# Kernel tuning notes

Measured on AMD Instinct MI355X. Metric: run time of the kernel, lower is better.

## Reference

```python
import jax, jax.numpy as jnp
import numpy as np

B, L, DM, H, DK, DV = 4, 1024, 1024, 16, 64, 64


def setup_inputs() -> dict:
    key = jax.random.key(0)
    ks = jax.random.split(key, 9)
    s = 0.02
    q = jax.random.normal(ks[0], (B, L, DM), jnp.float32)
    k = jax.random.normal(ks[1], (B, L, DM), jnp.float32)
    v = jax.random.normal(ks[2], (B, L, DM), jnp.float32)
    # causal mask: True = masked out
    attn_mask = jnp.broadcast_to(jnp.triu(jnp.ones((L, L), bool), k=1), (B, L, L))
    w_q = jax.random.normal(ks[3], (DM, H * DK), jnp.float32) * s
    w_k = jax.random.normal(ks[4], (DM, H * DK), jnp.float32) * s
    w_v = jax.random.normal(ks[5], (DM, H * DV), jnp.float32) * s
    w_o = jax.random.normal(ks[6], (H * DV, DM), jnp.float32) * s
    ln_g = jnp.ones((DM,), jnp.float32)
    ln_b = jnp.zeros((DM,), jnp.float32)
    return {"q": q, "k": k, "v": v, "w_q": w_q, "w_k": w_k, "w_v": w_v,
            "w_o": w_o, "ln_g": ln_g, "ln_b": ln_b,
            "attn_mask": attn_mask, "n_head": H}


def _mha(q, k, v, w_q, w_k, w_v, w_o, ln_g, ln_b, attn_mask, n_head):
    b, lq, dm = q.shape
    lk = k.shape[1]
    d_k = w_q.shape[1] // n_head
    d_v = w_v.shape[1] // n_head
    temper = jnp.asarray(np.sqrt(dm), q.dtype)  # NOTE: sqrt(d_model), as in source
    residual = q
    # faithful to source: flat .view reshape (b, l, h*d) -> (b*h, l, d), NO transpose
    qh = (q @ w_q).reshape(b * n_head, lq, d_k)
    kh = (k @ w_k).reshape(b * n_head, lk, d_k)
    vh = (v @ w_v).reshape(b * n_head, lk, d_v)
    attn = jnp.einsum('bqd,bkd->bqk', qh, kh) / temper  # (b*h, lq, lk)
    mask_r = jnp.tile(attn_mask, (n_head, 1, 1))
    attn = jnp.where(mask_r, -jnp.inf, attn)
    attn = jax.nn.softmax(attn, axis=-1)
    out = jnp.einsum('bqk,bkd->bqd', attn, vh)  # (b*h, lq, d_v)
    out = out.reshape(b, lq, n_head * d_v)
    out = out @ w_o + residual  # dropout = identity (eval)
    mu = jnp.mean(out, axis=-1, keepdims=True)
    var = jnp.mean(jnp.square(out - mu), axis=-1, keepdims=True)
    out = (out - mu) * jax.lax.rsqrt(var + 1e-6) * ln_g + ln_b
    return out, attn


def reference(q, k, v, w_q, w_k, w_v, w_o, ln_g, ln_b, attn_mask, n_head):
    return _mha(q, k, v, w_q, w_k, w_v, w_o, ln_g, ln_b, attn_mask, n_head)
```

## Files before the change

### kernel.cpp

```cpp
#include <hip/hip_runtime.h>
#include <stdint.h>

typedef unsigned short u16;
typedef __attribute__((ext_vector_type(8))) short bf16x8;
typedef __attribute__((ext_vector_type(4))) float f32x4;
typedef __attribute__((ext_vector_type(4))) unsigned short us4;

#define MFMA_BF16(a, b, c) __builtin_amdgcn_mfma_f32_16x16x32_bf16((a), (b), (c), 0, 0, 0)

__device__ __forceinline__ u16 f2bf(float f) {
  uint32_t u = __builtin_bit_cast(uint32_t, f);
  u += 0x7fffu + ((u >> 16) & 1u);
  return (u16)(u >> 16);
}

__device__ __forceinline__ void async_copy16(void* lds, const void* g) {
  __builtin_amdgcn_global_load_lds(
      (const __attribute__((address_space(1))) unsigned int*)g,
      (__attribute__((address_space(3))) unsigned int*)lds, 16, 0, 0);
}

__global__ __launch_bounds__(256) void k_cast3(const float4* __restrict__ q,
                                               const float4* __restrict__ k,
                                               const float4* __restrict__ v,
                                               us4* __restrict__ dst) {
  const float4* src = (blockIdx.y == 0) ? q : ((blockIdx.y == 1) ? k : v);
  int i = blockIdx.x * 256 + threadIdx.x;
  float4 val = src[i];
  us4 o;
  o[0] = f2bf(val.x); o[1] = f2bf(val.y); o[2] = f2bf(val.z); o[3] = f2bf(val.w);
  dst[(size_t)blockIdx.y * 1048576 + i] = o;
}

__global__ __launch_bounds__(256) void k_wtrans4(const float* __restrict__ w0,
                                                 const float* __restrict__ w1,
                                                 const float* __restrict__ w2,
                                                 const float* __restrict__ w3,
                                                 u16* __restrict__ dstbase) {
  const float* W = (blockIdx.z == 0) ? w0 : (blockIdx.z == 1) ? w1
                   : (blockIdx.z == 2) ? w2 : w3;
  u16* WT = dstbase + (size_t)blockIdx.z * 1048576;
  __shared__ float t[32][33];
  int bx = blockIdx.x, by = blockIdx.y;
  int tid = threadIdx.x;
  int c = tid & 31, r0 = tid >> 5;
#pragma unroll
  for (int i = 0; i < 4; ++i) {
    int r = r0 + i * 8;
    t[r][c] = W[(size_t)(by * 32 + r) * 1024 + bx * 32 + c];
  }
  __syncthreads();
#pragma unroll
  for (int i = 0; i < 4; ++i) {
    int r = r0 + i * 8;
    WT[(size_t)(bx * 32 + r) * 1024 + by * 32 + c] = f2bf(t[c][r]);
  }
}

__global__ __launch_bounds__(256) void k_vtrans(const u16* __restrict__ VP, u16* __restrict__ VT) {
  int jt = blockIdx.x;
  int bh = blockIdx.y;
  __shared__ u16 t[64][65];
  int tid = threadIdx.x;
  const u16* src = VP + (size_t)bh * 65536 + (size_t)jt * 64 * 64;
#pragma unroll
  for (int i = 0; i < 16; ++i) {
    int e = tid + i * 256;
    t[e >> 6][e & 63] = src[e];
  }
  __syncthreads();
  u16* dst = VT + (size_t)bh * 65536 + jt * 64;
#pragma unroll
  for (int i = 0; i < 16; ++i) {
    int e = tid + i * 256;
    int d = e >> 6, j = e & 63;
    dst[(size_t)d * 1024 + j] = t[j][d];
  }
}

__global__ __launch_bounds__(256) void k_gemm_bt(const u16* __restrict__ A,
                                                 const u16* __restrict__ BT,
                                                 u16* __restrict__ Cb, float* __restrict__ Cf,
                                                 const float* __restrict__ res,
                                                 int N, int K, int mode, int wgrp) {
  __shared__ __align__(16) u16 As[2][4096];
  __shared__ __align__(16) u16 Bs[2][4096];
  int bm, bn;
  {
    int wg = blockIdx.x + blockIdx.y * gridDim.x;
    int per = gridDim.y >> 3;
    int xcd = wg & 7;
    int idx = wg >> 3;
    bm = xcd * per + (idx % per);
    bn = idx / per;
  }
  int tid = threadIdx.x;
  int wave = tid >> 6, lane = tid & 63;
  int wr = wave >> 1, wc = wave & 1;
  int fl = lane & 15, fg = lane >> 4;
  f32x4 acc[4][4] = {};

  const char* Abase = (const char*)(A + (size_t)bm * 128 * K);
  const char* Bbase = (const char*)(BT + (wgrp ? (size_t)(bm >> 5) * 1048576 : 0) +
                                    (size_t)bn * 128 * K);
  int off = wave * 1024 + lane * 16;

#define GSTAGE(buf, kt)                                                              \
  {                                                                                  \
    _Pragma("unroll") for (int is = 0; is < 2; ++is) {                               \
      int o = is * 4096 + off;                                                       \
      int row = o >> 6, cb = o & 63;                                                 \
      async_copy16((char*)As[buf] + is * 4096 + wave * 1024,                         \
                   Abase + (size_t)row * (K * 2) + (kt) * 2 + cb);                   \
      async_copy16((char*)Bs[buf] + is * 4096 + wave * 1024,                         \
                   Bbase + (size_t)row * (K * 2) + (kt) * 2 + cb);                   \
    }                                                                                \
  }

  GSTAGE(0, 0);
  __syncthreads();
  int cur = 0;
  for (int kt = 0; kt < K; kt += 32) {
    if (kt + 32 < K) GSTAGE(cur ^ 1, kt + 32);
    bf16x8 af[4], bfr[4];
#pragma unroll
    for (int m = 0; m < 4; ++m)
      af[m] = *(const bf16x8*)((const char*)As[cur] + (wr * 64 + m * 16 + fl) * 64 + fg * 16);
#pragma unroll
    for (int n = 0; n < 4; ++n)
      bfr[n] = *(const bf16x8*)((const char*)Bs[cur] + (wc * 64 + n * 16 + fl) * 64 + fg * 16);
#pragma unroll
    for (int m = 0; m < 4; ++m)
#pragma unroll
      for (int n = 0; n < 4; ++n)
        acc[m][n] = MFMA_BF16(af[m], bfr[n], acc[m][n]);
    __syncthreads();
    cur ^= 1;
  }
#undef GSTAGE

#pragma unroll
  for (int m = 0; m < 4; ++m)
#pragma unroll
    for (int n = 0; n < 4; ++n)
#pragma unroll
      for (int r = 0; r < 4; ++r) {
        int row = bm * 128 + wr * 64 + m * 16 + fg * 4 + r;
        int col = bn * 128 + wc * 64 + n * 16 + fl;
        float v = acc[m][n][r];
        if (mode)
          Cf[(size_t)row * N + col] = v + res[(size_t)row * N + col];
        else
          Cb[(size_t)row * N + col] = f2bf(v);
      }
}

__global__ __launch_bounds__(256) void k_attn(const u16* __restrict__ QP,
                                              const u16* __restrict__ KP,
                                              const u16* __restrict__ VT,
                                              float* __restrict__ attn,
                                              u16* __restrict__ AO) {
  int bh = blockIdx.x;
  int qb = 15 - blockIdx.y;
  int tid = threadIdx.x;
  int wave = tid >> 6, lane = tid & 63;
  int fl = lane & 15, fg = lane >> 4;
  int qw = qb * 64 + wave * 16;

  const u16* Qb = QP + (size_t)bh * 65536;
  const char* Kbyte = (const char*)(KP + (size_t)bh * 65536);
  const u16* Vb = VT + (size_t)bh * 65536;
  float* Ab = attn + (size_t)bh * 1048576;

  __shared__ __align__(16) u16 Ks[2][4096];
  __shared__ __align__(16) float Ps[4][16][68];
  __shared__ __align__(16) u16 Pt[4][16][64];

#define KSTAGE(buf, jt)                                                               \
  {                                                                                   \
    _Pragma("unroll") for (int c2 = 0; c2 < 2; ++c2) {                                \
      int o = c2 * 4096 + wave * 1024 + lane * 16;                                    \
      int row = o >> 7, col = o & 127;                                                \
      async_copy16((char*)Ks[buf] + c2 * 4096 + wave * 1024,                          \
                   Kbyte + (size_t)((jt) * 64 + row) * 128 + (col ^ ((row & 7) << 4))); \
    }                                                                                 \
  }

  bf16x8 qf0 = *(const bf16x8*)(Qb + (size_t)(qw + fl) * 64 + fg * 8);
  bf16x8 qf1 = *(const bf16x8*)(Qb + (size_t)(qw + fl) * 64 + 32 + fg * 8);

  float den[4] = {0.f, 0.f, 0.f, 0.f};

  KSTAGE(0, 0);
  __syncthreads();
  int cur = 0;
  for (int jt = 0; jt <= qb; ++jt) {
    if (jt < qb) KSTAGE(cur ^ 1, jt + 1);
    int j0 = jt * 64;
    f32x4 c[4] = {};
#pragma unroll
    for (int n = 0; n < 4; ++n) {
      int r = n * 16 + fl;
      bf16x8 k0 = *(const bf16x8*)((const char*)Ks[cur] + r * 128 + ((fg * 16) ^ ((r & 7) << 4)));
      bf16x8 k1 = *(const bf16x8*)((const char*)Ks[cur] + r * 128 + ((64 + fg * 16) ^ ((r & 7) << 4)));
      c[n] = MFMA_BF16(qf0, k0, c[n]);
      c[n] = MFMA_BF16(qf1, k1, c[n]);
    }
#pragma unroll
    for (int r = 0; r < 4; ++r) {
      int row = qw + fg * 4 + r;
      float sum = 0.f;
#pragma unroll
      for (int n = 0; n < 4; ++n) {
        int col = j0 + n * 16 + fl;
        float e = (col > row) ? 0.f : __expf(c[n][r] * 0.03125f);
        sum += e;
      }
#pragma unroll
      for (int o2 = 1; o2 < 16; o2 <<= 1) sum += __shfl_xor(sum, o2);
      den[r] += sum;
    }
    __syncthreads();
    cur ^= 1;
  }

  float invden[4];
#pragma unroll
  for (int r = 0; r < 4; ++r) invden[r] = 1.0f / den[r];

  f32x4 oacc[4] = {};

  KSTAGE(0, 0);
  __syncthreads();
  cur = 0;
  for (int jt = 0; jt <= qb; ++jt) {
    if (jt < qb) KSTAGE(cur ^ 1, jt + 1);
    int j0 = jt * 64;
    f32x4 c[4] = {};
#pragma unroll
    for (int n = 0; n < 4; ++n) {
      int r = n * 16 + fl;
      bf16x8 k0 = *(const bf16x8*)((const char*)Ks[cur] + r * 128 + ((fg * 16) ^ ((r & 7) << 4)));
      bf16x8 k1 = *(const bf16x8*)((const char*)Ks[cur] + r * 128 + ((64 + fg * 16) ^ ((r & 7) << 4)));
      c[n] = MFMA_BF16(qf0, k0, c[n]);
      c[n] = MFMA_BF16(qf1, k1, c[n]);
    }
#pragma unroll
    for (int r = 0; r < 4; ++r) {
      int row = qw + fg * 4 + r;
      int lr = fg * 4 + r;
#pragma unroll
      for (int n = 0; n < 4; ++n) {
        int col = j0 + n * 16 + fl;
        float p = (col > row) ? 0.f : __expf(c[n][r] * 0.03125f) * invden[r];
        Ps[wave][lr][n * 16 + fl] = p;
        Pt[wave][lr][n * 16 + fl] = f2bf(p);
      }
    }
    bf16x8 pa0 = *(const bf16x8*)(&Pt[wave][fl][fg * 8]);
    bf16x8 pa1 = *(const bf16x8*)(&Pt[wave][fl][32 + fg * 8]);
#pragma unroll
    for (int n = 0; n < 4; ++n) {
      const u16* vp = Vb + (size_t)(n * 16 + fl) * 1024 + j0;
      bf16x8 v0 = *(const bf16x8*)(vp + fg * 8);
      bf16x8 v1 = *(const bf16x8*)(vp + 32 + fg * 8);
      oacc[n] = MFMA_BF16(pa0, v0, oacc[n]);
      oacc[n] = MFMA_BF16(pa1, v1, oacc[n]);
    }
#pragma unroll
    for (int i = 0; i < 4; ++i) {
      int idx = i * 64 + lane;
      int r16 = idx >> 4, f4 = idx & 15;
      float4 val = *(const float4*)(&Ps[wave][r16][f4 * 4]);
      *(float4*)(Ab + (size_t)(qw + r16) * 1024 + j0 + f4 * 4) = val;
    }
    __syncthreads();
    cur ^= 1;
  }
#undef KSTAGE

  float4 z; z.x = 0.f; z.y = 0.f; z.z = 0.f; z.w = 0.f;
  for (int jt = qb + 1; jt < 16; ++jt) {
    int j0 = jt * 64;
#pragma unroll
    for (int i = 0; i < 4; ++i) {
      int idx = i * 64 + lane;
      int r16 = idx >> 4, f4 = idx & 15;
      *(float4*)(Ab + (size_t)(qw + r16) * 1024 + j0 + f4 * 4) = z;
    }
  }

#pragma unroll
  for (int n = 0; n < 4; ++n)
#pragma unroll
    for (int r = 0; r < 4; ++r)
      AO[(size_t)bh * 65536 + (size_t)(qw + fg * 4 + r) * 64 + n * 16 + fl] = f2bf(oacc[n][r]);
}

__global__ __launch_bounds__(256) void k_lnorm(float* __restrict__ io,
                                               const float* __restrict__ g,
                                               const float* __restrict__ b) {
  int row = blockIdx.x, tid = threadIdx.x;
  float* p = io + (size_t)row * 1024 + tid * 4;
  float4 x = *(const float4*)p;
  float s1 = x.x + x.y + x.z + x.w;
  float s2 = x.x * x.x + x.y * x.y + x.z * x.z + x.w * x.w;
#pragma unroll
  for (int o = 1; o < 64; o <<= 1) {
    s1 += __shfl_xor(s1, o);
    s2 += __shfl_xor(s2, o);
  }
  __shared__ float r1[4], r2[4];
  int wave = tid >> 6;
  if ((tid & 63) == 0) { r1[wave] = s1; r2[wave] = s2; }
  __syncthreads();
  s1 = r1[0] + r1[1] + r1[2] + r1[3];
  s2 = r2[0] + r2[1] + r2[2] + r2[3];
  float mu = s1 * (1.0f / 1024.0f);
  float var = s2 * (1.0f / 1024.0f) - mu * mu;
  float rs = rsqrtf(var + 1e-6f);
  float4 gg = *(const float4*)(g + tid * 4);
  float4 bb = *(const float4*)(b + tid * 4);
  float4 y;
  y.x = (x.x - mu) * rs * gg.x + bb.x;
  y.y = (x.y - mu) * rs * gg.y + bb.y;
  y.z = (x.z - mu) * rs * gg.z + bb.z;
  y.w = (x.w - mu) * rs * gg.w + bb.w;
  *(float4*)p = y;
}

extern "C" void kernel_launch(void* const* d_in, const int* in_sizes, int n_in,
                              void* d_out, int out_size, void* d_ws, size_t ws_size,
                              hipStream_t stream) {
  const float* q = (const float*)d_in[0];
  const float* k = (const float*)d_in[1];
  const float* v = (const float*)d_in[2];
  const float* w_q = (const float*)d_in[3];
  const float* w_k = (const float*)d_in[4];
  const float* w_v = (const float*)d_in[5];
  const float* w_o = (const float*)d_in[6];
  const float* ln_g = (const float*)d_in[7];
  const float* ln_b = (const float*)d_in[8];

  float* out = (float*)d_out;
  float* attnp = out + 4194304;

  char* ws = (char*)d_ws;
  u16* QP = (u16*)(ws);
  u16* VP = (u16*)(ws + (16u << 20));
  u16* VT = (u16*)(ws + (24u << 20));
  u16* AO = (u16*)(ws + (32u << 20));
  u16* wT = (u16*)(ws + (40u << 20));
  u16* KP = QP + 4194304;
  u16* woT = wT + 3145728;

  u16* qkvb = (u16*)attnp;

  k_cast3<<<dim3(4096, 3), 256, 0, stream>>>((const float4*)q, (const float4*)k,
                                             (const float4*)v, (us4*)qkvb);
  k_wtrans4<<<dim3(32, 32, 4), 256, 0, stream>>>(w_q, w_k, w_v, w_o, wT);

  k_gemm_bt<<<dim3(8, 96), 256, 0, stream>>>(qkvb, wT, QP, nullptr, nullptr, 1024, 1024, 0, 1);

  k_vtrans<<<dim3(16, 64), 256, 0, stream>>>(VP, VT);

  k_attn<<<dim3(64, 16), 256, 0, stream>>>(QP, KP, VT, attnp, AO);

  k_gemm_bt<<<dim3(8, 32), 256, 0, stream>>>(AO, woT, nullptr, out, q, 1024, 1024, 1, 0);

  k_lnorm<<<4096, 256, 0, stream>>>(out, ln_g, ln_b);
}
```

Baseline: 192.3 us.

## Fuse cast and weight transpose kernels, stage GEMM/attention epilogues through LDS for wide stores

Merges the activation cast and weight transpose into one launch, removing one kernel launch. Reworks the GEMM epilogue to stage accumulators in shared memory (reusing the operand buffers) so output, residual reads and bf16 stores become vectorized float4/8-wide coalesced accesses. The attention kernel shrinks its fp32 probability staging buffer, writing the attn matrix in two half-tile passes interleaved with the compute, and stages the output tile via LDS for 16-byte stores. These trade extra LDS traffic and a few wave-local LDS round-trips for fewer, wider global transactions.

```diff
diff --git a/kernel.cpp b/kernel.cpp
--- a/kernel.cpp
+++ b/kernel.cpp
@@ -20,40 +20,44 @@
       (__attribute__((address_space(3))) unsigned int*)lds, 16, 0, 0);
 }
 
-__global__ __launch_bounds__(256) void k_cast3(const float4* __restrict__ q,
-                                               const float4* __restrict__ k,
-                                               const float4* __restrict__ v,
-                                               us4* __restrict__ dst) {
-  const float4* src = (blockIdx.y == 0) ? q : ((blockIdx.y == 1) ? k : v);
-  int i = blockIdx.x * 256 + threadIdx.x;
-  float4 val = src[i];
-  us4 o;
-  o[0] = f2bf(val.x); o[1] = f2bf(val.y); o[2] = f2bf(val.z); o[3] = f2bf(val.w);
-  dst[(size_t)blockIdx.y * 1048576 + i] = o;
-}
-
-__global__ __launch_bounds__(256) void k_wtrans4(const float* __restrict__ w0,
-                                                 const float* __restrict__ w1,
-                                                 const float* __restrict__ w2,
-                                                 const float* __restrict__ w3,
-                                                 u16* __restrict__ dstbase) {
-  const float* W = (blockIdx.z == 0) ? w0 : (blockIdx.z == 1) ? w1
-                   : (blockIdx.z == 2) ? w2 : w3;
-  u16* WT = dstbase + (size_t)blockIdx.z * 1048576;
+__global__ __launch_bounds__(256) void k_pre(const float* __restrict__ q,
+                                             const float* __restrict__ k,
+                                             const float* __restrict__ v,
+                                             const float* __restrict__ w0,
+                                             const float* __restrict__ w1,
+                                             const float* __restrict__ w2,
+                                             const float* __restrict__ w3,
+                                             us4* __restrict__ qkvb,
+                                             u16* __restrict__ wT) {
   __shared__ float t[32][33];
-  int bx = blockIdx.x, by = blockIdx.y;
+  int bid = blockIdx.x;
   int tid = threadIdx.x;
-  int c = tid & 31, r0 = tid >> 5;
-#pragma unroll
-  for (int i = 0; i < 4; ++i) {
-    int r = r0 + i * 8;
-    t[r][c] = W[(size_t)(by * 32 + r) * 1024 + bx * 32 + c];
-  }
-  __syncthreads();
-#pragma unroll
-  for (int i = 0; i < 4; ++i) {
-    int r = r0 + i * 8;
-    WT[(size_t)(bx * 32 + r) * 1024 + by * 32 + c] = f2bf(t[c][r]);
+  if (bid < 12288) {
+    int z = bid >> 12;
+    const float4* src = (z == 0) ? (const float4*)q : (z == 1) ? (const float4*)k : (const float4*)v;
+    int i = (bid & 4095) * 256 + tid;
+    float4 val = src[i];
+    us4 o;
+    o[0] = f2bf(val.x); o[1] = f2bf(val.y); o[2] = f2bf(val.z); o[3] = f2bf(val.w);
+    qkvb[(size_t)z * 1048576 + i] = o;
+  } else {
+    int w = bid - 12288;
+    int z = w >> 10, r_ = w & 1023;
+    int bx = r_ & 31, by = r_ >> 5;
+    const float* W = (z == 0) ? w0 : (z == 1) ? w1 : (z == 2) ? w2 : w3;
+    u16* WT = wT + (size_t)z * 1048576;
+    int c = tid & 31, r0 = tid >> 5;
+#pragma unroll
+    for (int i = 0; i < 4; ++i) {
+      int r = r0 + i * 8;
+      t[r][c] = W[(size_t)(by * 32 + r) * 1024 + bx * 32 + c];
+    }
+    __syncthreads();
+#pragma unroll
+    for (int i = 0; i < 4; ++i) {
+      int r = r0 + i * 8;
+      WT[(size_t)(bx * 32 + r) * 1024 + by * 32 + c] = f2bf(t[c][r]);
+    }
   }
 }
 
@@ -83,8 +87,7 @@
                                                  u16* __restrict__ Cb, float* __restrict__ Cf,
                                                  const float* __restrict__ res,
                                                  int N, int K, int mode, int wgrp) {
-  __shared__ __align__(16) u16 As[2][4096];
-  __shared__ __align__(16) u16 Bs[2][4096];
+  __shared__ __align__(16) u16 SM[4][4096];
   int bm, bn;
   {
     int wg = blockIdx.x + blockIdx.y * gridDim.x;
@@ -110,9 +113,9 @@
     _Pragma("unroll") for (int is = 0; is < 2; ++is) {                               \
       int o = is * 4096 + off;                                                       \
       int row = o >> 6, cb = o & 63;                                                 \
-      async_copy16((char*)As[buf] + is * 4096 + wave * 1024,                         \
+      async_copy16((char*)SM[buf] + is * 4096 + wave * 1024,                         \
                    Abase + (size_t)row * (K * 2) + (kt) * 2 + cb);                   \
-      async_copy16((char*)Bs[buf] + is * 4096 + wave * 1024,                         \
+      async_copy16((char*)SM[2 + (buf)] + is * 4096 + wave * 1024,                   \
                    Bbase + (size_t)row * (K * 2) + (kt) * 2 + cb);                   \
     }                                                                                \
   }
@@ -125,10 +128,10 @@
     bf16x8 af[4], bfr[4];
 #pragma unroll
     for (int m = 0; m < 4; ++m)
-      af[m] = *(const bf16x8*)((const char*)As[cur] + (wr * 64 + m * 16 + fl) * 64 + fg * 16);
+      af[m] = *(const bf16x8*)((const char*)SM[cur] + (wr * 64 + m * 16 + fl) * 64 + fg * 16);
 #pragma unroll
     for (int n = 0; n < 4; ++n)
-      bfr[n] = *(const bf16x8*)((const char*)Bs[cur] + (wc * 64 + n * 16 + fl) * 64 + fg * 16);
+      bfr[n] = *(const bf16x8*)((const char*)SM[2 + cur] + (wc * 64 + n * 16 + fl) * 64 + fg * 16);
 #pragma unroll
     for (int m = 0; m < 4; ++m)
 #pragma unroll
@@ -139,20 +142,42 @@
   }
 #undef GSTAGE
 
-#pragma unroll
-  for (int m = 0; m < 4; ++m)
+  float* EP = (float*)&SM[0][0] + wave * 2048;
+  int colbase = bn * 128 + wc * 64;
+#pragma unroll
+  for (int m = 0; m < 4; ++m) {
+    int rowbase = bm * 128 + wr * 64 + m * 16;
 #pragma unroll
     for (int n = 0; n < 4; ++n)
 #pragma unroll
-      for (int r = 0; r < 4; ++r) {
-        int row = bm * 128 + wr * 64 + m * 16 + fg * 4 + r;
-        int col = bn * 128 + wc * 64 + n * 16 + fl;
-        float v = acc[m][n][r];
-        if (mode)
-          Cf[(size_t)row * N + col] = v + res[(size_t)row * N + col];
-        else
-          Cb[(size_t)row * N + col] = f2bf(v);
+      for (int r = 0; r < 4; ++r)
+        EP[(fg * 4 + r) * 68 + n * 16 + fl] = acc[m][n][r];
+    if (mode) {
+#pragma unroll
+      for (int j = 0; j < 4; ++j) {
+        int row = (lane >> 4) + 4 * j;
+        int colf = (lane & 15) * 4;
+        float4 val = *(const float4*)(&EP[row * 68 + colf]);
+        size_t gidx = (size_t)(rowbase + row) * N + colbase + colf;
+        float4 rr = *(const float4*)(res + gidx);
+        val.x += rr.x; val.y += rr.y; val.z += rr.z; val.w += rr.w;
+        *(float4*)(Cf + gidx) = val;
       }
+    } else {
+#pragma unroll
+      for (int j = 0; j < 2; ++j) {
+        int row = (lane >> 3) + 8 * j;
+        int colf = (lane & 7) * 8;
+        const float* s = &EP[row * 68 + colf];
+        us4 lo, hi;
+#pragma unroll
+        for (int i = 0; i < 4; ++i) { lo[i] = f2bf(s[i]); hi[i] = f2bf(s[4 + i]); }
+        u16* d = Cb + (size_t)(rowbase + row) * N + colbase + colf;
+        *(us4*)d = lo;
+        *(us4*)(d + 4) = hi;
+      }
+    }
+  }
 }
 
 __global__ __launch_bounds__(256) void k_attn(const u16* __restrict__ QP,
@@ -173,17 +198,17 @@
   float* Ab = attn + (size_t)bh * 1048576;
 
   __shared__ __align__(16) u16 Ks[2][4096];
-  __shared__ __align__(16) float Ps[4][16][68];
+  __shared__ __align__(16) float Ps[4][16][36];
   __shared__ __align__(16) u16 Pt[4][16][64];
 
-#define KSTAGE(buf, jt)                                                               \
-  {                                                                                   \
-    _Pragma("unroll") for (int c2 = 0; c2 < 2; ++c2) {                                \
-      int o = c2 * 4096 + wave * 1024 + lane * 16;                                    \
-      int row = o >> 7, col = o & 127;                                                \
-      async_copy16((char*)Ks[buf] + c2 * 4096 + wave * 1024,                          \
+#define KSTAGE(buf, jt)                                                                 \
+  {                                                                                     \
+    _Pragma("unroll") for (int c2 = 0; c2 < 2; ++c2) {                                  \
+      int o = c2 * 4096 + wave * 1024 + lane * 16;                                      \
+      int row = o >> 7, col = o & 127;                                                  \
+      async_copy16((char*)Ks[buf] + c2 * 4096 + wave * 1024,                            \
                    Kbyte + (size_t)((jt) * 64 + row) * 128 + (col ^ ((row & 7) << 4))); \
-    }                                                                                 \
+    }                                                                                   \
   }
 
   bf16x8 qf0 = *(const bf16x8*)(Qb + (size_t)(qw + fl) * 64 + fg * 8);
@@ -213,8 +238,7 @@
 #pragma unroll
       for (int n = 0; n < 4; ++n) {
         int col = j0 + n * 16 + fl;
-        float e = (col > row) ? 0.f : __expf(c[n][r] * 0.03125f);
-        sum += e;
+        sum += (col > row) ? 0.f : __expf(c[n][r] * 0.03125f);
       }
 #pragma unroll
       for (int o2 = 1; o2 < 16; o2 <<= 1) sum += __shfl_xor(sum, o2);
@@ -245,18 +269,36 @@
       c[n] = MFMA_BF16(qf0, k0, c[n]);
       c[n] = MFMA_BF16(qf1, k1, c[n]);
     }
+    float pv_[4][4];
 #pragma unroll
     for (int r = 0; r < 4; ++r) {
       int row = qw + fg * 4 + r;
-      int lr = fg * 4 + r;
 #pragma unroll
       for (int n = 0; n < 4; ++n) {
         int col = j0 + n * 16 + fl;
-        float p = (col > row) ? 0.f : __expf(c[n][r] * 0.03125f) * invden[r];
-        Ps[wave][lr][n * 16 + fl] = p;
-        Pt[wave][lr][n * 16 + fl] = f2bf(p);
+        pv_[n][r] = (col > row) ? 0.f : __expf(c[n][r] * 0.03125f) * invden[r];
       }
     }
+#pragma unroll
+    for (int t = 0; t < 2; ++t) {
+#pragma unroll
+      for (int n2 = 0; n2 < 2; ++n2)
+#pragma unroll
+        for (int r = 0; r < 4; ++r)
+          Ps[wave][fg * 4 + r][n2 * 16 + fl] = pv_[t * 2 + n2][r];
+#pragma unroll
+      for (int i = 0; i < 2; ++i) {
+        int idx = i * 64 + lane;
+        int r16 = idx >> 3, f4 = idx & 7;
+        float4 val = *(const float4*)(&Ps[wave][r16][f4 * 4]);
+        *(float4*)(Ab + (size_t)(qw + r16) * 1024 + j0 + t * 32 + f4 * 4) = val;
+      }
+    }
+#pragma unroll
+    for (int r = 0; r < 4; ++r)
+#pragma unroll
+      for (int n = 0; n < 4; ++n)
+        Pt[wave][fg * 4 + r][n * 16 + fl] = f2bf(pv_[n][r]);
     bf16x8 pa0 = *(const bf16x8*)(&Pt[wave][fl][fg * 8]);
     bf16x8 pa1 = *(const bf16x8*)(&Pt[wave][fl][32 + fg * 8]);
 #pragma unroll
@@ -267,13 +309,6 @@
       oacc[n] = MFMA_BF16(pa0, v0, oacc[n]);
       oacc[n] = MFMA_BF16(pa1, v1, oacc[n]);
     }
-#pragma unroll
-    for (int i = 0; i < 4; ++i) {
-      int idx = i * 64 + lane;
-      int r16 = idx >> 4, f4 = idx & 15;
-      float4 val = *(const float4*)(&Ps[wave][r16][f4 * 4]);
-      *(float4*)(Ab + (size_t)(qw + r16) * 1024 + j0 + f4 * 4) = val;
-    }
     __syncthreads();
     cur ^= 1;
   }
@@ -294,7 +329,14 @@
   for (int n = 0; n < 4; ++n)
 #pragma unroll
     for (int r = 0; r < 4; ++r)
-      AO[(size_t)bh * 65536 + (size_t)(qw + fg * 4 + r) * 64 + n * 16 + fl] = f2bf(oacc[n][r]);
+      Pt[wave][fg * 4 + r][n * 16 + fl] = f2bf(oacc[n][r]);
+#pragma unroll
+  for (int j = 0; j < 2; ++j) {
+    int row = (lane >> 3) + 8 * j;
+    int colf = (lane & 7) * 8;
+    bf16x8 val = *(const bf16x8*)(&Pt[wave][row][colf]);
+    *(bf16x8*)(AO + (size_t)bh * 65536 + (size_t)(qw + row) * 64 + colf) = val;
+  }
 }
 
 __global__ __launch_bounds__(256) void k_lnorm(float* __restrict__ io,
@@ -356,9 +398,7 @@
 
   u16* qkvb = (u16*)attnp;
 
-  k_cast3<<<dim3(4096, 3), 256, 0, stream>>>((const float4*)q, (const float4*)k,
-                                             (const float4*)v, (us4*)qkvb);
-  k_wtrans4<<<dim3(32, 32, 4), 256, 0, stream>>>(w_q, w_k, w_v, w_o, wT);
+  k_pre<<<16384, 256, 0, stream>>>(q, k, v, w_q, w_k, w_v, w_o, (us4*)qkvb, wT);
 
   k_gemm_bt<<<dim3(8, 96), 256, 0, stream>>>(qkvb, wT, QP, nullptr, nullptr, 1024, 1024, 0, 1);
 
```

After: 170.5 us. 11.3% less time.
